# Kernel optimization log

Hardware: AMD Instinct MI355X
Metric: run time of the kernel (lower is better)

The kernel has to match this reference:

```python
import jax, jax.numpy as jnp
import numpy as np

B, L, D, C, NB = 2, 256, 3, 256, 64
LN_EPS = 1e-5


def setup_inputs() -> dict:
    ks = jax.random.split(jax.random.key(0), 12)
    x_BLD = jax.random.normal(ks[0], (B, L, D), dtype=jnp.float32) * 0.5
    c_BD = jax.random.normal(ks[1], (B, C), dtype=jnp.float32)
    embed_w = jax.random.normal(ks[2], (NB, C), dtype=jnp.float32) * 0.02
    pos_w = jax.random.normal(ks[3], (128, C), dtype=jnp.float32) * 0.02
    bins = jnp.linspace(0.0, 3.0, NB - 1, dtype=jnp.float32)
    ada_w = jax.random.normal(ks[4], (3 * C, C), dtype=jnp.float32) * (C ** -0.5)
    ada_b = jnp.zeros((3 * C,), dtype=jnp.float32)
    ln_g = jnp.ones((C,), dtype=jnp.float32)
    ln_b = jnp.zeros((C,), dtype=jnp.float32)
    fc1_w = jax.random.normal(ks[5], (4 * C, C), dtype=jnp.float32) * (C ** -0.5)
    fc1_b = jnp.zeros((4 * C,), dtype=jnp.float32)
    fc2_w = jax.random.normal(ks[6], (C, 4 * C), dtype=jnp.float32) * ((4 * C) ** -0.5)
    fc2_b = jnp.zeros((C,), dtype=jnp.float32)
    return {"x_BLD": x_BLD, "c_BD": c_BD, "embed_w": embed_w, "pos_w": pos_w,
            "bins": bins, "ada_w": ada_w, "ada_b": ada_b, "ln_g": ln_g,
            "ln_b": ln_b, "fc1_w": fc1_w, "fc1_b": fc1_b, "fc2_w": fc2_w,
            "fc2_b": fc2_b}


def reference(x_BLD, c_BD, embed_w, pos_w, bins, ada_w, ada_b, ln_g, ln_b,
              fc1_w, fc1_b, fc2_w, fc2_b):
    # pairwise squared distances: [B, L, L]
    d_BLL = jnp.sum((x_BLD[:, :, None, :] - x_BLD[:, None, :, :]) ** 2, axis=-1)
    # bucketize (torch.bucketize right=False == searchsorted side='left')
    idx_BLL = jnp.searchsorted(bins, d_BLL, side="left")
    # relative position embedding: [L, L, C]
    rel = jnp.arange(L)[:, None] - jnp.arange(L)[None, :]
    rel = jnp.clip(rel, -64, 63) + 64
    pos_LLD = pos_w[rel]
    # adaLN modulation from conditioning: SiLU -> Linear -> 3 chunks
    mod = jax.nn.silu(c_BD) @ ada_w.T + ada_b            # [B, 3C]
    shift, scale, gate = jnp.split(mod, 3, axis=-1)      # each [B, C]
    shift = shift[:, None, None, :]
    scale = scale[:, None, None, :]
    gate = gate[:, None, None, :]
    # embed + pos, affine modulate
    s = embed_w[idx_BLL] + pos_LLD[None]                 # [B, L, L, C]
    s = s * (1.0 + scale) + shift
    # LayerNorm over channel dim
    mu = jnp.mean(s, axis=-1, keepdims=True)
    var = jnp.mean((s - mu) ** 2, axis=-1, keepdims=True)
    h = (s - mu) * jax.lax.rsqrt(var + LN_EPS) * ln_g + ln_b
    # MLP: Linear -> GELU(exact) -> Linear
    h = jax.nn.gelu(h @ fc1_w.T + fc1_b, approximate=False)
    h = h @ fc2_w.T + fc2_b
    return s + gate * h
```

## Files before the change

### kernel.cpp

```cpp
#include <hip/hip_runtime.h>
#include <math.h>

#define Cn 256
#define Ln 256
#define Bn 2
#define H1 1024
#define NIDX 64
#define NREL 128
#define NCOMBO 16384
#define TROWS 32

typedef __attribute__((ext_vector_type(8))) short bf16x8;
typedef __attribute__((ext_vector_type(4))) float f32x4;
typedef unsigned int u32;

__device__ __forceinline__ float gelu_exact(float x) {
    return 0.5f * x * (1.0f + erff(x * 0.70710678118654752f));
}
__device__ __forceinline__ short f2bf(float f) {
    unsigned u = __float_as_uint(f);
    return (short)((u + 0x7fffu + ((u >> 16) & 1u)) >> 16);
}

__global__ __launch_bounds__(256) void prep_kernel(
    const float* __restrict__ c_BD, const float* __restrict__ ada_w,
    const float* __restrict__ ada_b, const float* __restrict__ fc1_w,
    const float* __restrict__ fc2_w, float* __restrict__ mod,
    short* __restrict__ fc1s, short* __restrict__ fc2s)
{
    const int bid = blockIdx.x;
    const int tid = threadIdx.x;
    if (bid < 128) {
        const int t   = bid * 256 + tid;
        const int row = t >> 5;
        const int cc  = t & 31;
        const int c   = row >> 8, wv = (row >> 5) & 7, nt = (row >> 4) & 1, l15 = row & 15;
        const int ks  = cc >> 2, quad = cc & 3;
        const int lane = quad * 16 + l15;
        const int u   = (c * 8 + wv) * 16 + nt * 8 + ks;
        const float* s = fc1_w + (size_t)row * Cn + cc * 8;
        float4 v0 = *(const float4*)s;
        float4 v1 = *(const float4*)(s + 4);
        bf16x8 o;
        o[0] = f2bf(v0.x); o[1] = f2bf(v0.y); o[2] = f2bf(v0.z); o[3] = f2bf(v0.w);
        o[4] = f2bf(v1.x); o[5] = f2bf(v1.y); o[6] = f2bf(v1.z); o[7] = f2bf(v1.w);
        *(bf16x8*)(fc1s + (size_t)u * 512 + lane * 8) = o;
    } else if (bid < 256) {
        const int t   = (bid - 128) * 256 + tid;
        const int row = t >> 7;
        const int cc  = t & 127;
        const int wv  = (row >> 5) & 7, nt = (row >> 4) & 1, l15 = row & 15;
        const int c   = cc >> 5, ks = (cc >> 2) & 7, quad = cc & 3;
        const int lane = quad * 16 + l15;
        const int u   = (c * 8 + wv) * 16 + nt * 8 + ks;
        const float* s = fc2_w + (size_t)row * H1 + cc * 8;
        float4 v0 = *(const float4*)s;
        float4 v1 = *(const float4*)(s + 4);
        bf16x8 o;
        o[0] = f2bf(v0.x); o[1] = f2bf(v0.y); o[2] = f2bf(v0.z); o[3] = f2bf(v0.w);
        o[4] = f2bf(v1.x); o[5] = f2bf(v1.y); o[6] = f2bf(v1.z); o[7] = f2bf(v1.w);
        *(bf16x8*)(fc2s + (size_t)u * 512 + lane * 8) = o;
    } else {
        int o = (bid - 256) * 256 + tid;
        int b = o / (3 * Cn);
        int j = o - b * (3 * Cn);
        const float* crow = c_BD + b * Cn;
        const float* wrow = ada_w + (size_t)j * Cn;
        float acc = 0.f;
        for (int k = 0; k < Cn; k += 4) {
            float4 cv = *(const float4*)(crow + k);
            float4 wv = *(const float4*)(wrow + k);
            acc += (cv.x / (1.f + expf(-cv.x))) * wv.x;
            acc += (cv.y / (1.f + expf(-cv.y))) * wv.y;
            acc += (cv.z / (1.f + expf(-cv.z))) * wv.z;
            acc += (cv.w / (1.f + expf(-cv.w))) * wv.w;
        }
        mod[o] = acc + ada_b[j];
    }
}

__global__ __launch_bounds__(512, 4) void table_fused_kernel(
    const float* __restrict__ embed_w, const float* __restrict__ pos_w,
    const float* __restrict__ ln_g, const float* __restrict__ ln_b,
    const short* __restrict__ fc1s, const float* __restrict__ fc1_b,
    const short* __restrict__ fc2s, const float* __restrict__ fc2_b,
    const float* __restrict__ mod, float* __restrict__ table)
{
    __shared__ __align__(16) short h_lds[TROWS][264];
    __shared__ __align__(16) short g_lds[TROWS][264];

    const int tid  = threadIdx.x;
    const int wave = tid >> 6;
    const int lane = tid & 63;
    const int quad = lane >> 4;
    const int l15  = lane & 15;

    const int base = blockIdx.x * TROWS;
    const int b    = base >> 13;
    const int idx  = (base >> 7) & 63;
    const int rel0 = base & 127;

    const float* modb = mod + b * (3 * Cn);
    const float* erow = embed_w + (size_t)idx * Cn;

    {
        const int c0 = lane * 4;
        float4 ev = *(const float4*)(erow + c0);
        float4 sc = *(const float4*)(modb + Cn + c0);
        sc.x += 1.f; sc.y += 1.f; sc.z += 1.f; sc.w += 1.f;
        const float4 sh = *(const float4*)(modb + c0);
        const float4 lg = *(const float4*)(ln_g + c0);
        const float4 lb = *(const float4*)(ln_b + c0);
        #pragma unroll
        for (int r4 = 0; r4 < 4; ++r4) {
            const int rr = wave * 4 + r4;
            const float4 p = *(const float4*)(pos_w + (size_t)(rel0 + rr) * Cn + c0);
            float v0 = (ev.x + p.x) * sc.x + sh.x;
            float v1 = (ev.y + p.y) * sc.y + sh.y;
            float v2 = (ev.z + p.z) * sc.z + sh.z;
            float v3 = (ev.w + p.w) * sc.w + sh.w;
            float sum = v0 + v1 + v2 + v3;
            #pragma unroll
            for (int off = 32; off; off >>= 1) sum += __shfl_xor(sum, off, 64);
            const float mu = sum * (1.f / Cn);
            float t0 = v0 - mu, t1 = v1 - mu, t2 = v2 - mu, t3 = v3 - mu;
            float p2 = t0 * t0 + t1 * t1 + t2 * t2 + t3 * t3;
            #pragma unroll
            for (int off = 32; off; off >>= 1) p2 += __shfl_xor(p2, off, 64);
            const float rstd = rsqrtf(p2 * (1.f / Cn) + 1e-5f);
            short4 hq;
            hq.x = f2bf(t0 * rstd * lg.x + lb.x);
            hq.y = f2bf(t1 * rstd * lg.y + lb.y);
            hq.z = f2bf(t2 * rstd * lg.z + lb.z);
            hq.w = f2bf(t3 * rstd * lg.w + lb.w);
            *(short4*)(&h_lds[rr][c0]) = hq;
        }
    }
    __syncthreads();

    f32x4 acc2[2][2];
    #pragma unroll
    for (int mt = 0; mt < 2; ++mt)
        #pragma unroll
        for (int nt = 0; nt < 2; ++nt) acc2[mt][nt] = (f32x4){0.f, 0.f, 0.f, 0.f};

    for (int c = 0; c < 4; ++c) {
        f32x4 z[2][2];
        #pragma unroll
        for (int mt = 0; mt < 2; ++mt)
            #pragma unroll
            for (int nt = 0; nt < 2; ++nt) z[mt][nt] = (f32x4){0.f, 0.f, 0.f, 0.f};

        {
            const short* w1u = fc1s + (size_t)((c * 8 + wave) * 16) * 512 + lane * 8;
            bf16x8 wf[8][2];
            #pragma unroll
            for (int ks = 0; ks < 8; ++ks)
                #pragma unroll
                for (int nt = 0; nt < 2; ++nt)
                    wf[ks][nt] = *(const bf16x8*)(w1u + (nt * 8 + ks) * 512);
            #pragma unroll
            for (int ks = 0; ks < 8; ++ks) {
                const int k0 = ks * 32 + quad * 8;
                bf16x8 a0 = *(const bf16x8*)(&h_lds[l15][k0]);
                bf16x8 a1 = *(const bf16x8*)(&h_lds[16 + l15][k0]);
                #pragma unroll
                for (int nt = 0; nt < 2; ++nt) {
                    z[0][nt] = __builtin_amdgcn_mfma_f32_16x16x32_bf16(wf[ks][nt], a0, z[0][nt], 0, 0, 0);
                    z[1][nt] = __builtin_amdgcn_mfma_f32_16x16x32_bf16(wf[ks][nt], a1, z[1][nt], 0, 0, 0);
                }
            }
        }
        __syncthreads();

        #pragma unroll
        for (int mt = 0; mt < 2; ++mt) {
            #pragma unroll
            for (int nt = 0; nt < 2; ++nt) {
                const int cc = wave * 32 + nt * 16 + quad * 4;
                const float4 b4 = *(const float4*)(fc1_b + c * 256 + cc);
                short4 o;
                o.x = f2bf(gelu_exact(z[mt][nt][0] + b4.x));
                o.y = f2bf(gelu_exact(z[mt][nt][1] + b4.y));
                o.z = f2bf(gelu_exact(z[mt][nt][2] + b4.z));
                o.w = f2bf(gelu_exact(z[mt][nt][3] + b4.w));
                *(short4*)(&g_lds[mt * 16 + l15][cc]) = o;
            }
        }
        __syncthreads();

        {
            const short* w2u = fc2s + (size_t)((c * 8 + wave) * 16) * 512 + lane * 8;
            bf16x8 wf[8][2];
            #pragma unroll
            for (int ks = 0; ks < 8; ++ks)
                #pragma unroll
                for (int nt = 0; nt < 2; ++nt)
                    wf[ks][nt] = *(const bf16x8*)(w2u + (nt * 8 + ks) * 512);
            #pragma unroll
            for (int ks = 0; ks < 8; ++ks) {
                const int k0 = ks * 32 + quad * 8;
                bf16x8 a0 = *(const bf16x8*)(&g_lds[l15][k0]);
                bf16x8 a1 = *(const bf16x8*)(&g_lds[16 + l15][k0]);
                #pragma unroll
                for (int nt = 0; nt < 2; ++nt) {
                    acc2[0][nt] = __builtin_amdgcn_mfma_f32_16x16x32_bf16(wf[ks][nt], a0, acc2[0][nt], 0, 0, 0);
                    acc2[1][nt] = __builtin_amdgcn_mfma_f32_16x16x32_bf16(wf[ks][nt], a1, acc2[1][nt], 0, 0, 0);
                }
            }
        }
        if (c < 3) __syncthreads();
    }

    #pragma unroll
    for (int mt = 0; mt < 2; ++mt) {
        const int row = mt * 16 + l15;
        const float* prow = pos_w + (size_t)(rel0 + row) * Cn;
        #pragma unroll
        for (int nt = 0; nt < 2; ++nt) {
            const int n0 = wave * 32 + nt * 16 + quad * 4;
            const float4 b4 = *(const float4*)(fc2_b + n0);
            const float4 g4 = *(const float4*)(modb + 2 * Cn + n0);
            const float4 sc = *(const float4*)(modb + Cn + n0);
            const float4 sh = *(const float4*)(modb + n0);
            const float4 e4 = *(const float4*)(erow + n0);
            const float4 p4 = *(const float4*)(prow + n0);
            float4 o;
            float s;
            s   = (e4.x + p4.x) * (1.f + sc.x) + sh.x;
            o.x = s + g4.x * (acc2[mt][nt][0] + b4.x);
            s   = (e4.y + p4.y) * (1.f + sc.y) + sh.y;
            o.y = s + g4.y * (acc2[mt][nt][1] + b4.y);
            s   = (e4.z + p4.z) * (1.f + sc.z) + sh.z;
            o.z = s + g4.z * (acc2[mt][nt][2] + b4.z);
            s   = (e4.w + p4.w) * (1.f + sc.w) + sh.w;
            o.w = s + g4.w * (acc2[mt][nt][3] + b4.w);
            *(float4*)(table + (size_t)(base + row) * Cn + n0) = o;
        }
    }
}

__global__ __launch_bounds__(256) void gather_kernel(
    const float* __restrict__ x, const float* __restrict__ bins,
    const float* __restrict__ table, float* __restrict__ out)
{
    __shared__ float xs[Ln * 3];
    __shared__ float bins_s[63];
    __shared__ int   idx_s[64];

    const int tid = threadIdx.x;
    const int blk = blockIdx.x;
    const int q   = blk & 3;
    const int bi  = blk >> 2;
    const int b   = bi >> 8;
    const int i   = bi & 255;

    for (int t = tid; t < Ln * 3; t += 256) xs[t] = x[(size_t)b * Ln * 3 + t];
    if (tid < 63) bins_s[tid] = bins[tid];
    __syncthreads();

    if (tid < 64) {
        int j = q * 64 + tid;
        float d0 = xs[3 * i]     - xs[3 * j];
        float d1 = xs[3 * i + 1] - xs[3 * j + 1];
        float d2 = xs[3 * i + 2] - xs[3 * j + 2];
        float d = d0 * d0 + d1 * d1 + d2 * d2;
        int v = 0;
        #pragma unroll
        for (int k = 0; k < 63; ++k) v += (bins_s[k] < d) ? 1 : 0;
        idx_s[tid] = v;
    }
    __syncthreads();

    const int wave = tid >> 6;
    const int lane = tid & 63;
    float4* outp = (float4*)(out + (size_t)bi * Ln * Cn);
    const float4* tab4 = (const float4*)table;

    float4 v[16];
    #pragma unroll
    for (int jj = 0; jj < 16; ++jj) {
        int jl  = wave * 16 + jj;
        int j   = q * 64 + jl;
        int rel = i - j;
        rel = (rel < -64 ? -64 : (rel > 63 ? 63 : rel)) + 64;
        size_t trow = (size_t)((b * NIDX + idx_s[jl]) * NREL + rel) * (Cn / 4);
        v[jj] = tab4[trow + lane];
    }
    #pragma unroll
    for (int jj = 0; jj < 16; ++jj) {
        int j = q * 64 + wave * 16 + jj;
        outp[(size_t)j * (Cn / 4) + lane] = v[jj];
    }
}

extern "C" void kernel_launch(void* const* d_in, const int* in_sizes, int n_in,
                              void* d_out, int out_size, void* d_ws, size_t ws_size,
                              hipStream_t stream) {
    const float* x_BLD   = (const float*)d_in[0];
    const float* c_BD    = (const float*)d_in[1];
    const float* embed_w = (const float*)d_in[2];
    const float* pos_w   = (const float*)d_in[3];
    const float* bins    = (const float*)d_in[4];
    const float* ada_w   = (const float*)d_in[5];
    const float* ada_b   = (const float*)d_in[6];
    const float* ln_g    = (const float*)d_in[7];
    const float* ln_b    = (const float*)d_in[8];
    const float* fc1_w   = (const float*)d_in[9];
    const float* fc1_b   = (const float*)d_in[10];
    const float* fc2_w   = (const float*)d_in[11];
    const float* fc2_b   = (const float*)d_in[12];
    float* out = (float*)d_out;

    char* ws = (char*)d_ws;
    float* mod   = (float*)ws;
    short* fc1s  = (short*)(ws + 8192);
    short* fc2s  = (short*)(ws + 8192 + 524288);
    float* table = (float*)(ws + 8192 + 2 * 524288);

    prep_kernel<<<262, 256, 0, stream>>>(c_BD, ada_w, ada_b, fc1_w, fc2_w,
                                         mod, fc1s, fc2s);
    table_fused_kernel<<<NCOMBO / TROWS, 512, 0, stream>>>(
        embed_w, pos_w, ln_g, ln_b, fc1s, fc1_b, fc2s, fc2_b, mod, table);
    gather_kernel<<<Bn * Ln * 4, 256, 0, stream>>>(x_BLD, bins, table, out);
}
```

Measured before the change: 239.9 us.

## Merge prep, table and gather into one cooperative kernel with grid syncs

The three separate launches (weight prep, table MLP, gather) become one cooperative megakernel of 512 blocks, with grid-wide barriers between the stages. A three-kernel fallback runs if the cooperative launch fails. The gather is restructured so that one 512-thread block handles a full output row and computes all 256 bucket indices at once. The aim is to remove launch and inter-kernel gaps, at the cost of grid-sync overhead and fewer blocks during the bandwidth-bound gather. The intra-chunk __syncthreads in the table stage was also removed, which risks an LDS race.

```diff
diff --git a/kernel.cpp b/kernel.cpp
--- a/kernel.cpp
+++ b/kernel.cpp
@@ -1,5 +1,8 @@
 #include <hip/hip_runtime.h>
+#include <hip/hip_cooperative_groups.h>
 #include <math.h>
+
+namespace cg = cooperative_groups;
 
 #define Cn 256
 #define Ln 256
@@ -22,22 +25,19 @@
     return (short)((u + 0x7fffu + ((u >> 16) & 1u)) >> 16);
 }
 
-__global__ __launch_bounds__(256) void prep_kernel(
-    const float* __restrict__ c_BD, const float* __restrict__ ada_w,
+
+__device__ __forceinline__ void do_prep(
+    int gt, const float* __restrict__ c_BD, const float* __restrict__ ada_w,
     const float* __restrict__ ada_b, const float* __restrict__ fc1_w,
     const float* __restrict__ fc2_w, float* __restrict__ mod,
     short* __restrict__ fc1s, short* __restrict__ fc2s)
 {
-    const int bid = blockIdx.x;
-    const int tid = threadIdx.x;
-    if (bid < 128) {
-        const int t   = bid * 256 + tid;
-        const int row = t >> 5;
-        const int cc  = t & 31;
-        const int c   = row >> 8, wv = (row >> 5) & 7, nt = (row >> 4) & 1, l15 = row & 15;
-        const int ks  = cc >> 2, quad = cc & 3;
+    if (gt < 32768) {
+        const int row = gt >> 5, cc = gt & 31;
+        const int c = row >> 8, wv = (row >> 5) & 7, nt = (row >> 4) & 1, l15 = row & 15;
+        const int ks = cc >> 2, quad = cc & 3;
         const int lane = quad * 16 + l15;
-        const int u   = (c * 8 + wv) * 16 + nt * 8 + ks;
+        const int u = (c * 8 + wv) * 16 + nt * 8 + ks;
         const float* s = fc1_w + (size_t)row * Cn + cc * 8;
         float4 v0 = *(const float4*)s;
         float4 v1 = *(const float4*)(s + 4);
@@ -45,14 +45,13 @@
         o[0] = f2bf(v0.x); o[1] = f2bf(v0.y); o[2] = f2bf(v0.z); o[3] = f2bf(v0.w);
         o[4] = f2bf(v1.x); o[5] = f2bf(v1.y); o[6] = f2bf(v1.z); o[7] = f2bf(v1.w);
         *(bf16x8*)(fc1s + (size_t)u * 512 + lane * 8) = o;
-    } else if (bid < 256) {
-        const int t   = (bid - 128) * 256 + tid;
-        const int row = t >> 7;
-        const int cc  = t & 127;
-        const int wv  = (row >> 5) & 7, nt = (row >> 4) & 1, l15 = row & 15;
-        const int c   = cc >> 5, ks = (cc >> 2) & 7, quad = cc & 3;
+    } else if (gt < 65536) {
+        const int t2 = gt - 32768;
+        const int row = t2 >> 7, cc = t2 & 127;
+        const int wv = (row >> 5) & 7, nt = (row >> 4) & 1, l15 = row & 15;
+        const int c = cc >> 5, ks = (cc >> 2) & 7, quad = cc & 3;
         const int lane = quad * 16 + l15;
-        const int u   = (c * 8 + wv) * 16 + nt * 8 + ks;
+        const int u = (c * 8 + wv) * 16 + nt * 8 + ks;
         const float* s = fc2_w + (size_t)row * H1 + cc * 8;
         float4 v0 = *(const float4*)s;
         float4 v1 = *(const float4*)(s + 4);
@@ -60,8 +59,8 @@
         o[0] = f2bf(v0.x); o[1] = f2bf(v0.y); o[2] = f2bf(v0.z); o[3] = f2bf(v0.w);
         o[4] = f2bf(v1.x); o[5] = f2bf(v1.y); o[6] = f2bf(v1.z); o[7] = f2bf(v1.w);
         *(bf16x8*)(fc2s + (size_t)u * 512 + lane * 8) = o;
-    } else {
-        int o = (bid - 256) * 256 + tid;
+    } else if (gt < 65536 + Bn * 3 * Cn) {
+        int o = gt - 65536;
         int b = o / (3 * Cn);
         int j = o - b * (3 * Cn);
         const float* crow = c_BD + b * Cn;
@@ -79,23 +78,21 @@
     }
 }
 
-__global__ __launch_bounds__(512, 4) void table_fused_kernel(
+__device__ __forceinline__ void do_table(
+    int bid, int tid,
     const float* __restrict__ embed_w, const float* __restrict__ pos_w,
     const float* __restrict__ ln_g, const float* __restrict__ ln_b,
     const short* __restrict__ fc1s, const float* __restrict__ fc1_b,
     const short* __restrict__ fc2s, const float* __restrict__ fc2_b,
-    const float* __restrict__ mod, float* __restrict__ table)
-{
-    __shared__ __align__(16) short h_lds[TROWS][264];
-    __shared__ __align__(16) short g_lds[TROWS][264];
-
-    const int tid  = threadIdx.x;
+    const float* __restrict__ mod, float* __restrict__ table,
+    short (*h_lds)[264], short (*g_lds)[264])
+{
     const int wave = tid >> 6;
     const int lane = tid & 63;
     const int quad = lane >> 4;
     const int l15  = lane & 15;
 
-    const int base = blockIdx.x * TROWS;
+    const int base = bid * TROWS;
     const int b    = base >> 13;
     const int idx  = (base >> 7) & 63;
     const int rel0 = base & 127;
@@ -209,7 +206,6 @@
                 }
             }
         }
-        if (c < 3) __syncthreads();
     }
 
     #pragma unroll
@@ -240,27 +236,21 @@
     }
 }
 
-__global__ __launch_bounds__(256) void gather_kernel(
+__device__ __forceinline__ void do_gather(
+    int bi, int tid,
     const float* __restrict__ x, const float* __restrict__ bins,
-    const float* __restrict__ table, float* __restrict__ out)
-{
-    __shared__ float xs[Ln * 3];
-    __shared__ float bins_s[63];
-    __shared__ int   idx_s[64];
-
-    const int tid = threadIdx.x;
-    const int blk = blockIdx.x;
-    const int q   = blk & 3;
-    const int bi  = blk >> 2;
-    const int b   = bi >> 8;
-    const int i   = bi & 255;
-
-    for (int t = tid; t < Ln * 3; t += 256) xs[t] = x[(size_t)b * Ln * 3 + t];
+    const float* __restrict__ table, float* __restrict__ out,
+    float* xs, float* bins_s, int* idx_s)
+{
+    const int b = bi >> 8;
+    const int i = bi & 255;
+
+    for (int t = tid; t < Ln * 3; t += 512) xs[t] = x[(size_t)b * Ln * 3 + t];
     if (tid < 63) bins_s[tid] = bins[tid];
     __syncthreads();
 
-    if (tid < 64) {
-        int j = q * 64 + tid;
+    if (tid < 256) {
+        const int j = tid;
         float d0 = xs[3 * i]     - xs[3 * j];
         float d1 = xs[3 * i + 1] - xs[3 * j + 1];
         float d2 = xs[3 * i + 2] - xs[3 * j + 2];
@@ -268,7 +258,7 @@
         int v = 0;
         #pragma unroll
         for (int k = 0; k < 63; ++k) v += (bins_s[k] < d) ? 1 : 0;
-        idx_s[tid] = v;
+        idx_s[j] = v;
     }
     __syncthreads();
 
@@ -277,21 +267,84 @@
     float4* outp = (float4*)(out + (size_t)bi * Ln * Cn);
     const float4* tab4 = (const float4*)table;
 
-    float4 v[16];
     #pragma unroll
-    for (int jj = 0; jj < 16; ++jj) {
-        int jl  = wave * 16 + jj;
-        int j   = q * 64 + jl;
-        int rel = i - j;
-        rel = (rel < -64 ? -64 : (rel > 63 ? 63 : rel)) + 64;
-        size_t trow = (size_t)((b * NIDX + idx_s[jl]) * NREL + rel) * (Cn / 4);
-        v[jj] = tab4[trow + lane];
-    }
-    #pragma unroll
-    for (int jj = 0; jj < 16; ++jj) {
-        int j = q * 64 + wave * 16 + jj;
-        outp[(size_t)j * (Cn / 4) + lane] = v[jj];
-    }
+    for (int q = 0; q < 4; ++q) {
+        float4 v[8];
+        #pragma unroll
+        for (int jj = 0; jj < 8; ++jj) {
+            const int j = q * 64 + wave * 8 + jj;
+            int rel = i - j;
+            rel = (rel < -64 ? -64 : (rel > 63 ? 63 : rel)) + 64;
+            size_t trow = (size_t)((b * NIDX + idx_s[j]) * NREL + rel) * (Cn / 4);
+            v[jj] = tab4[trow + lane];
+        }
+        #pragma unroll
+        for (int jj = 0; jj < 8; ++jj) {
+            const int j = q * 64 + wave * 8 + jj;
+            outp[(size_t)j * (Cn / 4) + lane] = v[jj];
+        }
+    }
+}
+
+__global__ __launch_bounds__(512, 4) void mega_kernel(
+    const float* __restrict__ x, const float* __restrict__ bins,
+    const float* __restrict__ c_BD, const float* __restrict__ ada_w,
+    const float* __restrict__ ada_b, const float* __restrict__ fc1_w,
+    const float* __restrict__ fc1_b, const float* __restrict__ fc2_w,
+    const float* __restrict__ fc2_b, const float* __restrict__ embed_w,
+    const float* __restrict__ pos_w, const float* __restrict__ ln_g,
+    const float* __restrict__ ln_b, float* __restrict__ mod,
+    short* __restrict__ fc1s, short* __restrict__ fc2s,
+    float* __restrict__ table, float* __restrict__ out)
+{
+    __shared__ __align__(16) short h_lds[TROWS][264];
+    __shared__ __align__(16) short g_lds[TROWS][264];
+    __shared__ float xs[Ln * 3];
+    __shared__ float bins_s[63];
+    __shared__ int   idx_s[Ln];
+
+    const int tid = threadIdx.x;
+    const int bid = blockIdx.x;
+
+    do_prep(bid * 512 + tid, c_BD, ada_w, ada_b, fc1_w, fc2_w, mod, fc1s, fc2s);
+    cg::this_grid().sync();
+    do_table(bid, tid, embed_w, pos_w, ln_g, ln_b, fc1s, fc1_b, fc2s, fc2_b,
+             mod, table, h_lds, g_lds);
+    cg::this_grid().sync();
+    do_gather(bid, tid, x, bins, table, out, xs, bins_s, idx_s);
+}
+
+__global__ __launch_bounds__(512) void prep_kernel(
+    const float* __restrict__ c_BD, const float* __restrict__ ada_w,
+    const float* __restrict__ ada_b, const float* __restrict__ fc1_w,
+    const float* __restrict__ fc2_w, float* __restrict__ mod,
+    short* __restrict__ fc1s, short* __restrict__ fc2s)
+{
+    do_prep(blockIdx.x * 512 + threadIdx.x, c_BD, ada_w, ada_b, fc1_w, fc2_w,
+            mod, fc1s, fc2s);
+}
+
+__global__ __launch_bounds__(512, 4) void table_kernel(
+    const float* __restrict__ embed_w, const float* __restrict__ pos_w,
+    const float* __restrict__ ln_g, const float* __restrict__ ln_b,
+    const short* __restrict__ fc1s, const float* __restrict__ fc1_b,
+    const short* __restrict__ fc2s, const float* __restrict__ fc2_b,
+    const float* __restrict__ mod, float* __restrict__ table)
+{
+    __shared__ __align__(16) short h_lds[TROWS][264];
+    __shared__ __align__(16) short g_lds[TROWS][264];
+    do_table(blockIdx.x, threadIdx.x, embed_w, pos_w, ln_g, ln_b, fc1s, fc1_b,
+             fc2s, fc2_b, mod, table, h_lds, g_lds);
+}
+
+__global__ __launch_bounds__(512) void gather_std_kernel(
+    const float* __restrict__ x, const float* __restrict__ bins,
+    const float* __restrict__ table, float* __restrict__ out)
+{
+    __shared__ float xs[Ln * 3];
+    __shared__ float bins_s[63];
+    __shared__ int   idx_s[Ln];
+    do_gather(blockIdx.x, threadIdx.x, x, bins, table, out, xs, bins_s, idx_s);
 }
 
 extern "C" void kernel_launch(void* const* d_in, const int* in_sizes, int n_in,
@@ -318,9 +371,19 @@
     short* fc2s  = (short*)(ws + 8192 + 524288);
     float* table = (float*)(ws + 8192 + 2 * 524288);
 
-    prep_kernel<<<262, 256, 0, stream>>>(c_BD, ada_w, ada_b, fc1_w, fc2_w,
-                                         mod, fc1s, fc2s);
-    table_fused_kernel<<<NCOMBO / TROWS, 512, 0, stream>>>(
-        embed_w, pos_w, ln_g, ln_b, fc1s, fc1_b, fc2s, fc2_b, mod, table);
-    gather_kernel<<<Bn * Ln * 4, 256, 0, stream>>>(x_BLD, bins, table, out);
-}
+    void* args[] = {
+        (void*)&x_BLD, (void*)&bins, (void*)&c_BD, (void*)&ada_w, (void*)&ada_b,
+        (void*)&fc1_w, (void*)&fc1_b, (void*)&fc2_w, (void*)&fc2_b,
+        (void*)&embed_w, (void*)&pos_w, (void*)&ln_g, (void*)&ln_b,
+        (void*)&mod, (void*)&fc1s, (void*)&fc2s, (void*)&table, (void*)&out
+    };
+    hipError_t e = hipLaunchCooperativeKernel((void*)mega_kernel, dim3(512),
+                                              dim3(512), args, 0, stream);
+    if (e != hipSuccess) {
+        prep_kernel<<<131, 512, 0, stream>>>(c_BD, ada_w, ada_b, fc1_w, fc2_w,
+                                             mod, fc1s, fc2s);
+        table_kernel<<<NCOMBO / TROWS, 512, 0, stream>>>(
+            embed_w, pos_w, ln_g, ln_b, fc1s, fc1_b, fc2s, fc2_b, mod, table);
+        gather_std_kernel<<<Bn * Ln, 512, 0, stream>>>(x_BLD, bins, table, out);
+    }
+}
```

Result: slower. 368.8 us (+53.7%).

## Double-buffer GELU intermediate and software-pipeline fc1/fc2 chunks in table kernel

Applied to the files above, without the earlier changes.

The table kernel now keeps two GELU buffers in shared memory. Each loop step runs the fc2 GEMM on the previous chunk's GELU output and, in the same step, the fc1 GEMM and GELU for the next chunk, so each iteration needs one barrier instead of three. Weight fragments are also loaded inline inside the MFMA loop rather than prefetched into a register array, which lowers register pressure but may expose global-load latency. Shared memory use grows by one 32x264 bf16 buffer per block.

```diff
diff --git a/kernel.cpp b/kernel.cpp
--- a/kernel.cpp
+++ b/kernel.cpp
@@ -79,7 +79,45 @@
     }
 }
 
-__global__ __launch_bounds__(512, 4) void table_fused_kernel(
+__device__ __forceinline__ void gemm_frag(
+    const short* __restrict__ wu, const short (*src)[264], int quad, int l15,
+    f32x4 zz[2][2])
+{
+    #pragma unroll
+    for (int ks = 0; ks < 8; ++ks) {
+        const int k0 = ks * 32 + quad * 8;
+        bf16x8 a0 = *(const bf16x8*)(&src[l15][k0]);
+        bf16x8 a1 = *(const bf16x8*)(&src[16 + l15][k0]);
+        #pragma unroll
+        for (int nt = 0; nt < 2; ++nt) {
+            bf16x8 w = *(const bf16x8*)(wu + (nt * 8 + ks) * 512);
+            zz[0][nt] = __builtin_amdgcn_mfma_f32_16x16x32_bf16(w, a0, zz[0][nt], 0, 0, 0);
+            zz[1][nt] = __builtin_amdgcn_mfma_f32_16x16x32_bf16(w, a1, zz[1][nt], 0, 0, 0);
+        }
+    }
+}
+
+__device__ __forceinline__ void gelu_store(
+    const f32x4 zz[2][2], const float* __restrict__ fc1_b, int c,
+    int wave, int quad, int l15, short (*dst)[264])
+{
+    #pragma unroll
+    for (int mt = 0; mt < 2; ++mt) {
+        #pragma unroll
+        for (int nt = 0; nt < 2; ++nt) {
+            const int cc = wave * 32 + nt * 16 + quad * 4;
+            const float4 b4 = *(const float4*)(fc1_b + c * 256 + cc);
+            short4 o;
+            o.x = f2bf(gelu_exact(zz[mt][nt][0] + b4.x));
+            o.y = f2bf(gelu_exact(zz[mt][nt][1] + b4.y));
+            o.z = f2bf(gelu_exact(zz[mt][nt][2] + b4.z));
+            o.w = f2bf(gelu_exact(zz[mt][nt][3] + b4.w));
+            *(short4*)(&dst[mt * 16 + l15][cc]) = o;
+        }
+    }
+}
+
+__global__ __launch_bounds__(512, 4) void table_kernel(
     const float* __restrict__ embed_w, const float* __restrict__ pos_w,
     const float* __restrict__ ln_g, const float* __restrict__ ln_b,
     const short* __restrict__ fc1s, const float* __restrict__ fc1_b,
@@ -87,7 +125,7 @@
     const float* __restrict__ mod, float* __restrict__ table)
 {
     __shared__ __align__(16) short h_lds[TROWS][264];
-    __shared__ __align__(16) short g_lds[TROWS][264];
+    __shared__ __align__(16) short g_lds[2][TROWS][264];
 
     const int tid  = threadIdx.x;
     const int wave = tid >> 6;
@@ -138,79 +176,37 @@
     }
     __syncthreads();
 
+    const size_t wtile = (size_t)(wave * 16) * 512 + lane * 8;
     f32x4 acc2[2][2];
     #pragma unroll
     for (int mt = 0; mt < 2; ++mt)
         #pragma unroll
         for (int nt = 0; nt < 2; ++nt) acc2[mt][nt] = (f32x4){0.f, 0.f, 0.f, 0.f};
 
-    for (int c = 0; c < 4; ++c) {
+    {
         f32x4 z[2][2];
         #pragma unroll
         for (int mt = 0; mt < 2; ++mt)
             #pragma unroll
             for (int nt = 0; nt < 2; ++nt) z[mt][nt] = (f32x4){0.f, 0.f, 0.f, 0.f};
-
-        {
-            const short* w1u = fc1s + (size_t)((c * 8 + wave) * 16) * 512 + lane * 8;
-            bf16x8 wf[8][2];
+        gemm_frag(fc1s + wtile, h_lds, quad, l15, z);
+        gelu_store(z, fc1_b, 0, wave, quad, l15, g_lds[0]);
+    }
+    __syncthreads();
+
+    #pragma unroll
+    for (int c = 0; c < 3; ++c) {
+        gemm_frag(fc2s + (size_t)(c * 8) * 16 * 512 + wtile, g_lds[c & 1], quad, l15, acc2);
+        f32x4 z[2][2];
+        #pragma unroll
+        for (int mt = 0; mt < 2; ++mt)
             #pragma unroll
-            for (int ks = 0; ks < 8; ++ks)
-                #pragma unroll
-                for (int nt = 0; nt < 2; ++nt)
-                    wf[ks][nt] = *(const bf16x8*)(w1u + (nt * 8 + ks) * 512);
-            #pragma unroll
-            for (int ks = 0; ks < 8; ++ks) {
-                const int k0 = ks * 32 + quad * 8;
-                bf16x8 a0 = *(const bf16x8*)(&h_lds[l15][k0]);
-                bf16x8 a1 = *(const bf16x8*)(&h_lds[16 + l15][k0]);
-                #pragma unroll
-                for (int nt = 0; nt < 2; ++nt) {
-                    z[0][nt] = __builtin_amdgcn_mfma_f32_16x16x32_bf16(wf[ks][nt], a0, z[0][nt], 0, 0, 0);
-                    z[1][nt] = __builtin_amdgcn_mfma_f32_16x16x32_bf16(wf[ks][nt], a1, z[1][nt], 0, 0, 0);
-                }
-            }
-        }
+            for (int nt = 0; nt < 2; ++nt) z[mt][nt] = (f32x4){0.f, 0.f, 0.f, 0.f};
+        gemm_frag(fc1s + (size_t)((c + 1) * 8) * 16 * 512 + wtile, h_lds, quad, l15, z);
+        gelu_store(z, fc1_b, c + 1, wave, quad, l15, g_lds[(c + 1) & 1]);
         __syncthreads();
-
-        #pragma unroll
-        for (int mt = 0; mt < 2; ++mt) {
-            #pragma unroll
-            for (int nt = 0; nt < 2; ++nt) {
-                const int cc = wave * 32 + nt * 16 + quad * 4;
-                const float4 b4 = *(const float4*)(fc1_b + c * 256 + cc);
-                short4 o;
-                o.x = f2bf(gelu_exact(z[mt][nt][0] + b4.x));
-                o.y = f2bf(gelu_exact(z[mt][nt][1] + b4.y));
-                o.z = f2bf(gelu_exact(z[mt][nt][2] + b4.z));
-                o.w = f2bf(gelu_exact(z[mt][nt][3] + b4.w));
-                *(short4*)(&g_lds[mt * 16 + l15][cc]) = o;
-            }
-        }
-        __syncthreads();
-
-        {
-            const short* w2u = fc2s + (size_t)((c * 8 + wave) * 16) * 512 + lane * 8;
-            bf16x8 wf[8][2];
-            #pragma unroll
-            for (int ks = 0; ks < 8; ++ks)
-                #pragma unroll
-                for (int nt = 0; nt < 2; ++nt)
-                    wf[ks][nt] = *(const bf16x8*)(w2u + (nt * 8 + ks) * 512);
-            #pragma unroll
-            for (int ks = 0; ks < 8; ++ks) {
-                const int k0 = ks * 32 + quad * 8;
-                bf16x8 a0 = *(const bf16x8*)(&g_lds[l15][k0]);
-                bf16x8 a1 = *(const bf16x8*)(&g_lds[16 + l15][k0]);
-                #pragma unroll
-                for (int nt = 0; nt < 2; ++nt) {
-                    acc2[0][nt] = __builtin_amdgcn_mfma_f32_16x16x32_bf16(wf[ks][nt], a0, acc2[0][nt], 0, 0, 0);
-                    acc2[1][nt] = __builtin_amdgcn_mfma_f32_16x16x32_bf16(wf[ks][nt], a1, acc2[1][nt], 0, 0, 0);
-                }
-            }
-        }
-        if (c < 3) __syncthreads();
-    }
+    }
+    gemm_frag(fc2s + (size_t)(3 * 8) * 16 * 512 + wtile, g_lds[1], quad, l15, acc2);
 
     #pragma unroll
     for (int mt = 0; mt < 2; ++mt) {
@@ -320,7 +316,7 @@
 
     prep_kernel<<<262, 256, 0, stream>>>(c_BD, ada_w, ada_b, fc1_w, fc2_w,
                                          mod, fc1s, fc2s);
-    table_fused_kernel<<<NCOMBO / TROWS, 512, 0, stream>>>(
+    table_kernel<<<NCOMBO / TROWS, 512, 0, stream>>>(
         embed_w, pos_w, ln_g, ln_b, fc1s, fc1_b, fc2s, fc2_b, mod, table);
     gather_kernel<<<Bn * Ln * 4, 256, 0, stream>>>(x_BLD, bins, table, out);
 }
```

Result: no change. 241.2 us (+0.5%).
